# Kernel optimization log

Hardware: AMD Instinct MI355X
Metric: run time of the kernel (lower is better)

## Reference

```python
import jax, jax.numpy as jnp
import numpy as np


def _squash_global(v):
    # Faithful to torch: v.norm() with no dim -> global Frobenius norm (scalar).
    n2 = jnp.sum(v * v)
    n = jnp.sqrt(n2)
    scale = n2 / (1.0 + n2)
    return scale * v / n


def setup_inputs() -> dict:
    key = jax.random.key(0)
    k1, k2 = jax.random.split(key)
    B, R, Ci = 128, 1152, 8
    C, O = 10, 16
    x = jax.random.normal(k1, (B, R, Ci), dtype=jnp.float32)
    W = jax.random.normal(k2, (C, R, Ci, O), dtype=jnp.float32)  # routing_weights ~ randn
    return {"x": x, "W": W, "num_iterations": 3}


def reference(x, W, num_iterations):
    # prediction_vectors: [C, B, R, 1, O]
    u = jnp.einsum('bri,crio->cbro', x, W)[:, :, :, None, :]
    logits = jnp.zeros_like(u)
    v = None
    for _ in range(num_iterations):
        # batch_softmax: cat over dim0 + legacy softmax(dim=1 of 4D) == softmax over
        # the num_route_nodes axis (axis 2 here).
        c = jax.nn.softmax(logits, axis=2)
        s = jnp.sum(c * u, axis=2, keepdims=True)  # [C, B, 1, 1, O]
        v = _squash_global(s)
        logits = logits + u * v
    return v
```

## Files before the change

### kernel.cpp

```cpp
#include <hip/hip_runtime.h>
#include <math.h>

#define Bn   128
#define Rn   1152
#define CIn  8
#define Cn   10
#define On   16
#define BO   2048
#define CBO  20480
#define RC   12
#define NSEG 96
#define PSEG 24

__global__ __launch_bounds__(256)
void transpose_x(const float* __restrict__ X, float* __restrict__ XT)
{
    const int r = blockIdx.x;
    const int b = threadIdx.x & 127;
    const int g = threadIdx.x >> 7;
    float4 v = *(const float4*)(X + (size_t)b * (Rn * CIn) + r * CIn + g * 4);
    ((float4*)XT)[r * 256 + g * 128 + b] = v;
}

template<int PASS>
__global__ __launch_bounds__(256, 3)
void pass_kernel(const float* __restrict__ XT, const float* __restrict__ W,
                 const float* __restrict__ Sprev, const float* __restrict__ N2,
                 float* __restrict__ PT, float* __restrict__ PL)
{
    __shared__ __align__(16) float smem[4 * 64 * 34];
    float (*wlds)[128] = (float (*)[128])smem;
    float (*red)[64][34] = (float (*)[64][34])smem;

    const int blk  = blockIdx.x;
    const int c    = blk / 48;
    const int rem  = blk - c * 48;
    const int bh   = rem / 24;
    const int segq = rem - bh * 24;
    const int tid  = threadIdx.x;
    const int w    = tid >> 6;
    const int lane = tid & 63;
    const int b    = bh * 64 + lane;

    {
        const float4* gw4 = (const float4*)(W + (size_t)(c * Rn + segq * 48) * 128);
        float4* sw4 = (float4*)&wlds[0][0];
        #pragma unroll
        for (int k = 0; k < 6; ++k)
            sw4[tid + k * 256] = gw4[tid + k * 256];
    }

    float vs[16];
    if (PASS > 1) {
        float coef[PASS];
        #pragma unroll
        for (int t = 0; t < PASS - 1; ++t) {
            const float n2 = N2[t];
            coef[t] = n2 / ((1.0f + n2) * sqrtf(n2)) * 1.4426950408889634f;
        }
        const float* sp = Sprev + c * BO + b * On;
        #pragma unroll
        for (int q = 0; q < 4; ++q) {
            float4 a = make_float4(0.f, 0.f, 0.f, 0.f);
            #pragma unroll
            for (int t = 0; t < PASS - 1; ++t) {
                const float4 s4 = *(const float4*)(sp + t * CBO + q * 4);
                a.x = fmaf(coef[t], s4.x, a.x);
                a.y = fmaf(coef[t], s4.y, a.y);
                a.z = fmaf(coef[t], s4.z, a.z);
                a.w = fmaf(coef[t], s4.w, a.w);
            }
            vs[q * 4 + 0] = a.x; vs[q * 4 + 1] = a.y;
            vs[q * 4 + 2] = a.z; vs[q * 4 + 3] = a.w;
        }
    }

    float tacc[16], lacc[16];
    #pragma unroll
    for (int o = 0; o < 16; ++o) { tacc[o] = 0.0f; lacc[o] = 0.0f; }

    __syncthreads();

    const float4* XT4 = (const float4*)XT;
    for (int rr = 0; rr < RC; ++rr) {
        const int lrow = w * RC + rr;
        const int r    = segq * 48 + lrow;
        const float4 xa = XT4[r * 256 + b];
        const float4 xb = XT4[r * 256 + 128 + b];
        const float xi[8] = { xa.x, xa.y, xa.z, xa.w, xb.x, xb.y, xb.z, xb.w };

        float u[16];
        #pragma unroll
        for (int o = 0; o < 16; ++o) u[o] = 0.0f;
        #pragma unroll
        for (int i = 0; i < 8; ++i) {
            const float4 w0 = *(const float4*)&wlds[lrow][i * 16 + 0];
            const float4 w1 = *(const float4*)&wlds[lrow][i * 16 + 4];
            const float4 w2 = *(const float4*)&wlds[lrow][i * 16 + 8];
            const float4 w3 = *(const float4*)&wlds[lrow][i * 16 + 12];
            const float x = xi[i];
            u[0]  = fmaf(x, w0.x, u[0]);  u[1]  = fmaf(x, w0.y, u[1]);
            u[2]  = fmaf(x, w0.z, u[2]);  u[3]  = fmaf(x, w0.w, u[3]);
            u[4]  = fmaf(x, w1.x, u[4]);  u[5]  = fmaf(x, w1.y, u[5]);
            u[6]  = fmaf(x, w1.z, u[6]);  u[7]  = fmaf(x, w1.w, u[7]);
            u[8]  = fmaf(x, w2.x, u[8]);  u[9]  = fmaf(x, w2.y, u[9]);
            u[10] = fmaf(x, w2.z, u[10]); u[11] = fmaf(x, w2.w, u[11]);
            u[12] = fmaf(x, w3.x, u[12]); u[13] = fmaf(x, w3.y, u[13]);
            u[14] = fmaf(x, w3.z, u[14]); u[15] = fmaf(x, w3.w, u[15]);
        }
        #pragma unroll
        for (int o = 0; o < 16; ++o) {
            if (PASS == 1) {
                tacc[o] += u[o];
            } else {
                const float e = exp2f(u[o] * vs[o]);
                lacc[o] += e;
                tacc[o] = fmaf(e, u[o], tacc[o]);
            }
        }
    }

    __syncthreads();

    #pragma unroll
    for (int o = 0; o < 16; ++o) {
        red[w][lane][o]      = tacc[o];
        red[w][lane][16 + o] = lacc[o];
    }
    __syncthreads();

    {
        const int bl = tid >> 2;
        const int og = tid & 3;
        const int bg = bh * 64 + bl;
        float4 tv, lv;
        float* tp = (float*)&tv;
        float* lp = (float*)&lv;
        #pragma unroll
        for (int q = 0; q < 4; ++q) {
            const int o = og * 4 + q;
            tp[q] = red[0][bl][o] + red[1][bl][o] + red[2][bl][o] + red[3][bl][o];
            lp[q] = red[0][bl][16 + o] + red[1][bl][16 + o] +
                    red[2][bl][16 + o] + red[3][bl][16 + o];
        }
        const int idx = segq * CBO + c * BO + bg * On + og * 4;
        *(float4*)(PT + idx) = tv;
        if (PASS > 1) *(float4*)(PL + idx) = lv;
    }
}

template<int PASS>
__global__ __launch_bounds__(256)
void combine_kernel(const float* __restrict__ PT, const float* __restrict__ PL,
                    float* __restrict__ Sout, float* __restrict__ n2out)
{
    const int i = blockIdx.x * 256 + threadIdx.x;
    float T = 0.0f, L = 0.0f;
    #pragma unroll
    for (int s = 0; s < PSEG; ++s) T += PT[s * CBO + i];
    if (PASS == 1) {
        L = (float)Rn;
    } else {
        #pragma unroll
        for (int s = 0; s < PSEG; ++s) L += PL[s * CBO + i];
    }
    const float sv = T / L;
    Sout[i] = sv;
    float sq = sv * sv;
    #pragma unroll
    for (int d = 1; d < 64; d <<= 1) sq += __shfl_xor(sq, d);
    __shared__ float red[4];
    if ((threadIdx.x & 63) == 0) red[threadIdx.x >> 6] = sq;
    __syncthreads();
    if (threadIdx.x == 0)
        atomicAdd(n2out, red[0] + red[1] + red[2] + red[3]);
}

__global__ __launch_bounds__(256)
void final_kernel(const float* __restrict__ S, const float* __restrict__ n2p,
                  float* __restrict__ out)
{
    const int i = blockIdx.x * 256 + threadIdx.x;
    const float n2 = *n2p;
    const float coef = n2 / ((1.0f + n2) * sqrtf(n2));
    out[i] = coef * S[i];
}

extern "C" void kernel_launch(void* const* d_in, const int* in_sizes, int n_in,
                              void* d_out, int out_size, void* d_ws, size_t ws_size,
                              hipStream_t stream)
{
    const float* X = (const float*)d_in[0];
    const float* W = (const float*)d_in[1];
    float* ws = (float*)d_ws;
    float* XT = ws;
    float* N2 = XT + Rn * Bn * CIn;
    float* PT = N2 + 4;
    float* PL = PT + PSEG * CBO;
    float* S  = PL + PSEG * CBO;

    hipMemsetAsync(N2, 0, 16, stream);

    transpose_x<<<Rn, 256, 0, stream>>>(X, XT);
    pass_kernel<1><<<480, 256, 0, stream>>>(XT, W, S, N2, PT, PL);
    combine_kernel<1><<<80, 256, 0, stream>>>(PT, PL, S + 0 * CBO, N2 + 0);
    pass_kernel<2><<<480, 256, 0, stream>>>(XT, W, S, N2, PT, PL);
    combine_kernel<2><<<80, 256, 0, stream>>>(PT, PL, S + 1 * CBO, N2 + 1);
    pass_kernel<3><<<480, 256, 0, stream>>>(XT, W, S, N2, PT, PL);
    combine_kernel<3><<<80, 256, 0, stream>>>(PT, PL, S + 2 * CBO, N2 + 2);
    final_kernel<<<80, 256, 0, stream>>>(S + 2 * CBO, N2 + 2, (float*)d_out);
}
```

Before: 125.7 us.

## Fuse all routing passes into one persistent kernel with grid barriers

Replaces the eight separate launches (transpose, three pass/combine pairs, final scale) with one persistent kernel of 240 blocks × 512 threads that uses atomic-counter grid barriers between phases. Each block now covers 96 routing rows with 8 waves, which halves the partial-sum segments and adds a two-step LDS reduction. The aim is to remove kernel launch gaps and tail effects. In exchange it relies on all 240 blocks being co-resident for the spin barriers, and only 40 blocks do work in the combine phases.

```diff
diff --git a/kernel.cpp b/kernel.cpp
--- a/kernel.cpp
+++ b/kernel.cpp
@@ -9,45 +9,47 @@
 #define BO   2048
 #define CBO  20480
 #define RC   12
-#define NSEG 96
-#define PSEG 24
-
-__global__ __launch_bounds__(256)
-void transpose_x(const float* __restrict__ X, float* __restrict__ XT)
-{
-    const int r = blockIdx.x;
-    const int b = threadIdx.x & 127;
-    const int g = threadIdx.x >> 7;
-    float4 v = *(const float4*)(X + (size_t)b * (Rn * CIn) + r * CIn + g * 4);
-    ((float4*)XT)[r * 256 + g * 128 + b] = v;
+#define PSEG 12
+#define GRID 240
+#define NTHR 512
+#define AGT  __HIP_MEMORY_SCOPE_AGENT
+
+__device__ __forceinline__ void gbar(unsigned* bar, int tid)
+{
+    __syncthreads();
+    if (tid == 0) {
+        __hip_atomic_fetch_add(bar, 1u, __ATOMIC_RELEASE, AGT);
+        while (__hip_atomic_load(bar, __ATOMIC_RELAXED, AGT) < (unsigned)GRID)
+            __builtin_amdgcn_s_sleep(2);
+    }
+    __syncthreads();
+    __builtin_amdgcn_fence(__ATOMIC_ACQUIRE, "agent");
 }
 
 template<int PASS>
-__global__ __launch_bounds__(256, 3)
-void pass_kernel(const float* __restrict__ XT, const float* __restrict__ W,
-                 const float* __restrict__ Sprev, const float* __restrict__ N2,
-                 float* __restrict__ PT, float* __restrict__ PL)
-{
-    __shared__ __align__(16) float smem[4 * 64 * 34];
-    float (*wlds)[128] = (float (*)[128])smem;
+__device__ __forceinline__ void pass_phase(
+    int blk, int tid,
+    const float* __restrict__ XT, const float* __restrict__ W,
+    const float* __restrict__ Sprev, float* __restrict__ N2,
+    float* __restrict__ PT, float* __restrict__ PL, float* smem)
+{
+    float (*wlds)[128]   = (float (*)[128])smem;
     float (*red)[64][34] = (float (*)[64][34])smem;
 
-    const int blk  = blockIdx.x;
-    const int c    = blk / 48;
-    const int rem  = blk - c * 48;
-    const int bh   = rem / 24;
-    const int segq = rem - bh * 24;
-    const int tid  = threadIdx.x;
+    const int c    = blk / 24;
+    const int rem  = blk - c * 24;
+    const int bh   = rem / 12;
+    const int segq = rem - bh * 12;
     const int w    = tid >> 6;
     const int lane = tid & 63;
     const int b    = bh * 64 + lane;
 
     {
-        const float4* gw4 = (const float4*)(W + (size_t)(c * Rn + segq * 48) * 128);
-        float4* sw4 = (float4*)&wlds[0][0];
+        const float4* gw4 = (const float4*)(W + (size_t)(c * Rn + segq * 96) * 128);
+        float4* sw4 = (float4*)smem;
         #pragma unroll
         for (int k = 0; k < 6; ++k)
-            sw4[tid + k * 256] = gw4[tid + k * 256];
+            sw4[tid + k * 512] = gw4[tid + k * 512];
     }
 
     float vs[16];
@@ -55,7 +57,7 @@
         float coef[PASS];
         #pragma unroll
         for (int t = 0; t < PASS - 1; ++t) {
-            const float n2 = N2[t];
+            const float n2 = __hip_atomic_load(&N2[t], __ATOMIC_RELAXED, AGT);
             coef[t] = n2 / ((1.0f + n2) * sqrtf(n2)) * 1.4426950408889634f;
         }
         const float* sp = Sprev + c * BO + b * On;
@@ -84,7 +86,7 @@
     const float4* XT4 = (const float4*)XT;
     for (int rr = 0; rr < RC; ++rr) {
         const int lrow = w * RC + rr;
-        const int r    = segq * 48 + lrow;
+        const int r    = segq * 96 + lrow;
         const float4 xa = XT4[r * 256 + b];
         const float4 xb = XT4[r * 256 + 128 + b];
         const float xi[8] = { xa.x, xa.y, xa.z, xa.w, xb.x, xb.y, xb.z, xb.w };
@@ -122,39 +124,49 @@
 
     __syncthreads();
 
-    #pragma unroll
-    for (int o = 0; o < 16; ++o) {
-        red[w][lane][o]      = tacc[o];
-        red[w][lane][16 + o] = lacc[o];
+    if (w < 4) {
+        #pragma unroll
+        for (int o = 0; o < 16; ++o) {
+            red[w][lane][o]      = tacc[o];
+            red[w][lane][16 + o] = lacc[o];
+        }
+    }
+    __syncthreads();
+    if (w >= 4) {
+        #pragma unroll
+        for (int o = 0; o < 16; ++o) {
+            red[w - 4][lane][o]      += tacc[o];
+            red[w - 4][lane][16 + o] += lacc[o];
+        }
     }
     __syncthreads();
 
     {
-        const int bl = tid >> 2;
-        const int og = tid & 3;
+        const int bl = tid >> 3;
+        const int og = tid & 7;
         const int bg = bh * 64 + bl;
-        float4 tv, lv;
+        float2 tv, lv;
         float* tp = (float*)&tv;
         float* lp = (float*)&lv;
         #pragma unroll
-        for (int q = 0; q < 4; ++q) {
-            const int o = og * 4 + q;
+        for (int q = 0; q < 2; ++q) {
+            const int o = og * 2 + q;
             tp[q] = red[0][bl][o] + red[1][bl][o] + red[2][bl][o] + red[3][bl][o];
             lp[q] = red[0][bl][16 + o] + red[1][bl][16 + o] +
                     red[2][bl][16 + o] + red[3][bl][16 + o];
         }
-        const int idx = segq * CBO + c * BO + bg * On + og * 4;
-        *(float4*)(PT + idx) = tv;
-        if (PASS > 1) *(float4*)(PL + idx) = lv;
+        const int idx = segq * CBO + c * BO + bg * On + og * 2;
+        *(float2*)(PT + idx) = tv;
+        if (PASS > 1) *(float2*)(PL + idx) = lv;
     }
 }
 
 template<int PASS>
-__global__ __launch_bounds__(256)
-void combine_kernel(const float* __restrict__ PT, const float* __restrict__ PL,
-                    float* __restrict__ Sout, float* __restrict__ n2out)
-{
-    const int i = blockIdx.x * 256 + threadIdx.x;
+__device__ __forceinline__ void combine_phase(
+    int blk, int tid, const float* __restrict__ PT, const float* __restrict__ PL,
+    float* __restrict__ Sout, float* __restrict__ n2out, float* smem)
+{
+    const int i = blk * NTHR + tid;
     float T = 0.0f, L = 0.0f;
     #pragma unroll
     for (int s = 0; s < PSEG; ++s) T += PT[s * CBO + i];
@@ -169,21 +181,59 @@
     float sq = sv * sv;
     #pragma unroll
     for (int d = 1; d < 64; d <<= 1) sq += __shfl_xor(sq, d);
-    __shared__ float red[4];
-    if ((threadIdx.x & 63) == 0) red[threadIdx.x >> 6] = sq;
-    __syncthreads();
-    if (threadIdx.x == 0)
-        atomicAdd(n2out, red[0] + red[1] + red[2] + red[3]);
-}
-
-__global__ __launch_bounds__(256)
-void final_kernel(const float* __restrict__ S, const float* __restrict__ n2p,
+    if ((tid & 63) == 0) smem[tid >> 6] = sq;
+    __syncthreads();
+    if (tid == 0) {
+        float s8 = 0.0f;
+        #pragma unroll
+        for (int k = 0; k < 8; ++k) s8 += smem[k];
+        atomicAdd(n2out, s8);
+    }
+}
+
+__global__ __launch_bounds__(NTHR, 1)
+void fused_kernel(const float* __restrict__ X, const float* __restrict__ W,
+                  float* __restrict__ XT, float* __restrict__ PT,
+                  float* __restrict__ PL, float* __restrict__ S,
+                  float* __restrict__ N2, unsigned* __restrict__ BAR,
                   float* __restrict__ out)
 {
-    const int i = blockIdx.x * 256 + threadIdx.x;
-    const float n2 = *n2p;
-    const float coef = n2 / ((1.0f + n2) * sqrtf(n2));
-    out[i] = coef * S[i];
+    __shared__ __align__(16) float smem[96 * 128];
+
+    const int blk = blockIdx.x;
+    const int tid = threadIdx.x;
+
+    for (int idx = blk * NTHR + tid; idx < Rn * 256; idx += GRID * NTHR) {
+        const int r = idx >> 8;
+        const int j = idx & 255;
+        const int b = j & 127;
+        const int g = j >> 7;
+        float4 v = *(const float4*)(X + (size_t)b * (Rn * CIn) + r * CIn + g * 4);
+        ((float4*)XT)[r * 256 + g * 128 + b] = v;
+    }
+    gbar(BAR + 0, tid);
+
+    pass_phase<1>(blk, tid, XT, W, S, N2, PT, PL, smem);
+    gbar(BAR + 1, tid);
+    if (blk < 40) combine_phase<1>(blk, tid, PT, PL, S + 0 * CBO, N2 + 0, smem);
+    gbar(BAR + 2, tid);
+
+    pass_phase<2>(blk, tid, XT, W, S, N2, PT, PL, smem);
+    gbar(BAR + 3, tid);
+    if (blk < 40) combine_phase<2>(blk, tid, PT, PL, S + 1 * CBO, N2 + 1, smem);
+    gbar(BAR + 4, tid);
+
+    pass_phase<3>(blk, tid, XT, W, S, N2, PT, PL, smem);
+    gbar(BAR + 5, tid);
+    if (blk < 40) combine_phase<3>(blk, tid, PT, PL, S + 2 * CBO, N2 + 2, smem);
+    gbar(BAR + 6, tid);
+
+    if (blk < 40) {
+        const int i = blk * NTHR + tid;
+        const float n2 = __hip_atomic_load(&N2[2], __ATOMIC_RELAXED, AGT);
+        const float coef = n2 / ((1.0f + n2) * sqrtf(n2));
+        out[i] = coef * S[2 * CBO + i];
+    }
 }
 
 extern "C" void kernel_launch(void* const* d_in, const int* in_sizes, int n_in,
@@ -193,20 +243,15 @@
     const float* X = (const float*)d_in[0];
     const float* W = (const float*)d_in[1];
     float* ws = (float*)d_ws;
-    float* XT = ws;
-    float* N2 = XT + Rn * Bn * CIn;
-    float* PT = N2 + 4;
-    float* PL = PT + PSEG * CBO;
-    float* S  = PL + PSEG * CBO;
-
-    hipMemsetAsync(N2, 0, 16, stream);
-
-    transpose_x<<<Rn, 256, 0, stream>>>(X, XT);
-    pass_kernel<1><<<480, 256, 0, stream>>>(XT, W, S, N2, PT, PL);
-    combine_kernel<1><<<80, 256, 0, stream>>>(PT, PL, S + 0 * CBO, N2 + 0);
-    pass_kernel<2><<<480, 256, 0, stream>>>(XT, W, S, N2, PT, PL);
-    combine_kernel<2><<<80, 256, 0, stream>>>(PT, PL, S + 1 * CBO, N2 + 1);
-    pass_kernel<3><<<480, 256, 0, stream>>>(XT, W, S, N2, PT, PL);
-    combine_kernel<3><<<80, 256, 0, stream>>>(PT, PL, S + 2 * CBO, N2 + 2);
-    final_kernel<<<80, 256, 0, stream>>>(S + 2 * CBO, N2 + 2, (float*)d_out);
-}
+    float* XT  = ws;
+    float* N2  = XT + Rn * Bn * CIn;
+    unsigned* BAR = (unsigned*)(N2 + 4);
+    float* PT  = N2 + 12;
+    float* PL  = PT + PSEG * CBO;
+    float* S   = PL + PSEG * CBO;
+    float* out = (float*)d_out;
+
+    hipMemsetAsync(N2, 0, 48, stream);
+
+    fused_kernel<<<GRID, NTHR, 0, stream>>>(X, W, XT, PT, PL, S, N2, BAR, out);
+}
```

Result: slower. 300.5 us (+139.1%).

## Fuse combine and final kernels into pass kernels via atomics and ticket

Applied to the files above, without the earlier changes.

The per-segment partial buffers and the separate combine and final kernels are replaced. Each pass block now atomically adds its reduced T/L sums straight into one global accumulator per pass. Each later pass recomputes the squared norms redundantly in every block, and the last block of pass 3 (chosen with a ticket counter) writes the squashed output. The memset is folded into the transpose kernel, and the x loads are software-prefetched one row ahead. This removes four launches and the partial-sum round trips, at the cost of atomic contention, a redundant 20K-element norm scan in every block, and a serial tail in the final block.

```diff
diff --git a/kernel.cpp b/kernel.cpp
--- a/kernel.cpp
+++ b/kernel.cpp
@@ -9,28 +9,41 @@
 #define BO   2048
 #define CBO  20480
 #define RC   12
-#define NSEG 96
-#define PSEG 24
+#define GRID 480
+#define LOG2E 1.4426950408889634f
+#define INV_R 8.6805555e-4f
+
 
 __global__ __launch_bounds__(256)
-void transpose_x(const float* __restrict__ X, float* __restrict__ XT)
+void transpose_x(const float* __restrict__ X, float* __restrict__ XT,
+                 float* __restrict__ TL)
 {
     const int r = blockIdx.x;
     const int b = threadIdx.x & 127;
     const int g = threadIdx.x >> 7;
     float4 v = *(const float4*)(X + (size_t)b * (Rn * CIn) + r * CIn + g * 4);
     ((float4*)XT)[r * 256 + g * 128 + b] = v;
+    const int zi = blockIdx.x * 256 + threadIdx.x;
+    if (zi < 25604) ((float4*)TL)[zi] = make_float4(0.f, 0.f, 0.f, 0.f);
 }
 
 template<int PASS>
-__global__ __launch_bounds__(256, 3)
+__global__ __launch_bounds__(256, 2)
 void pass_kernel(const float* __restrict__ XT, const float* __restrict__ W,
-                 const float* __restrict__ Sprev, const float* __restrict__ N2,
-                 float* __restrict__ PT, float* __restrict__ PL)
+                 float* __restrict__ TL, float* __restrict__ out)
 {
     __shared__ __align__(16) float smem[4 * 64 * 34];
-    float (*wlds)[128] = (float (*)[128])smem;
+    __shared__ float sred[8];
+    __shared__ int sdone;
+    float (*wlds)[128]   = (float (*)[128])smem;
     float (*red)[64][34] = (float (*)[64][34])smem;
+
+    float* T1 = TL;
+    float* T2 = TL + CBO;
+    float* L2 = TL + 2 * CBO;
+    float* T3 = TL + 3 * CBO;
+    float* L3 = TL + 4 * CBO;
+    unsigned* ticket = (unsigned*)(TL + 5 * CBO);
 
     const int blk  = blockIdx.x;
     const int c    = blk / 48;
@@ -44,7 +57,7 @@
 
     {
         const float4* gw4 = (const float4*)(W + (size_t)(c * Rn + segq * 48) * 128);
-        float4* sw4 = (float4*)&wlds[0][0];
+        float4* sw4 = (float4*)smem;
         #pragma unroll
         for (int k = 0; k < 6; ++k)
             sw4[tid + k * 256] = gw4[tid + k * 256];
@@ -52,26 +65,59 @@
 
     float vs[16];
     if (PASS > 1) {
-        float coef[PASS];
-        #pragma unroll
-        for (int t = 0; t < PASS - 1; ++t) {
-            const float n2 = N2[t];
-            coef[t] = n2 / ((1.0f + n2) * sqrtf(n2)) * 1.4426950408889634f;
-        }
-        const float* sp = Sprev + c * BO + b * On;
-        #pragma unroll
-        for (int q = 0; q < 4; ++q) {
-            float4 a = make_float4(0.f, 0.f, 0.f, 0.f);
+        float n2a = 0.f, n2b = 0.f;
+        const float4* T1v = (const float4*)T1;
+        if (PASS == 2) {
+            for (int i = tid; i < 5120; i += 256) {
+                float4 v = T1v[i];
+                v.x *= INV_R; v.y *= INV_R; v.z *= INV_R; v.w *= INV_R;
+                n2a += v.x * v.x + v.y * v.y + v.z * v.z + v.w * v.w;
+            }
+        } else {
+            const float4* T2v = (const float4*)T2;
+            const float4* L2v = (const float4*)L2;
+            for (int i = tid; i < 5120; i += 256) {
+                float4 v = T1v[i];
+                v.x *= INV_R; v.y *= INV_R; v.z *= INV_R; v.w *= INV_R;
+                n2a += v.x * v.x + v.y * v.y + v.z * v.z + v.w * v.w;
+                float4 t = T2v[i], l = L2v[i];
+                float s0 = t.x / l.x, s1 = t.y / l.y, s2 = t.z / l.z, s3 = t.w / l.w;
+                n2b += s0 * s0 + s1 * s1 + s2 * s2 + s3 * s3;
+            }
+        }
+        #pragma unroll
+        for (int d = 1; d < 64; d <<= 1) {
+            n2a += __shfl_xor(n2a, d);
+            n2b += __shfl_xor(n2b, d);
+        }
+        if (lane == 0) { sred[w] = n2a; sred[4 + w] = n2b; }
+        __syncthreads();
+        n2a = sred[0] + sred[1] + sred[2] + sred[3];
+        n2b = sred[4] + sred[5] + sred[6] + sred[7];
+
+        const float c1 = n2a / ((1.f + n2a) * sqrtf(n2a)) * (LOG2E * INV_R);
+        const float* s1p = T1 + c * BO + b * On;
+        if (PASS == 2) {
             #pragma unroll
-            for (int t = 0; t < PASS - 1; ++t) {
-                const float4 s4 = *(const float4*)(sp + t * CBO + q * 4);
-                a.x = fmaf(coef[t], s4.x, a.x);
-                a.y = fmaf(coef[t], s4.y, a.y);
-                a.z = fmaf(coef[t], s4.z, a.z);
-                a.w = fmaf(coef[t], s4.w, a.w);
-            }
-            vs[q * 4 + 0] = a.x; vs[q * 4 + 1] = a.y;
-            vs[q * 4 + 2] = a.z; vs[q * 4 + 3] = a.w;
+            for (int q = 0; q < 4; ++q) {
+                float4 v = *(const float4*)(s1p + q * 4);
+                vs[q*4+0] = c1 * v.x; vs[q*4+1] = c1 * v.y;
+                vs[q*4+2] = c1 * v.z; vs[q*4+3] = c1 * v.w;
+            }
+        } else {
+            const float c2 = n2b / ((1.f + n2b) * sqrtf(n2b)) * LOG2E;
+            const float* t2p = T2 + c * BO + b * On;
+            const float* l2p = L2 + c * BO + b * On;
+            #pragma unroll
+            for (int q = 0; q < 4; ++q) {
+                float4 v = *(const float4*)(s1p + q * 4);
+                float4 t = *(const float4*)(t2p + q * 4);
+                float4 l = *(const float4*)(l2p + q * 4);
+                vs[q*4+0] = c1 * v.x + c2 * (t.x / l.x);
+                vs[q*4+1] = c1 * v.y + c2 * (t.y / l.y);
+                vs[q*4+2] = c1 * v.z + c2 * (t.z / l.z);
+                vs[q*4+3] = c1 * v.w + c2 * (t.w / l.w);
+            }
         }
     }
 
@@ -82,11 +128,16 @@
     __syncthreads();
 
     const float4* XT4 = (const float4*)XT;
+    const float4* xp  = XT4 + (size_t)(segq * 48 + w * RC) * 256 + b;
+    float4 xa = xp[0];
+    float4 xb = xp[128];
     for (int rr = 0; rr < RC; ++rr) {
+        float4 na = xa, nb = xb;
+        if (rr + 1 < RC) {
+            na = xp[(rr + 1) * 256];
+            nb = xp[(rr + 1) * 256 + 128];
+        }
         const int lrow = w * RC + rr;
-        const int r    = segq * 48 + lrow;
-        const float4 xa = XT4[r * 256 + b];
-        const float4 xb = XT4[r * 256 + 128 + b];
         const float xi[8] = { xa.x, xa.y, xa.z, xa.w, xb.x, xb.y, xb.z, xb.w };
 
         float u[16];
@@ -118,14 +169,15 @@
                 tacc[o] = fmaf(e, u[o], tacc[o]);
             }
         }
+        xa = na; xb = nb;
     }
 
     __syncthreads();
 
     #pragma unroll
     for (int o = 0; o < 16; ++o) {
-        red[w][lane][o]      = tacc[o];
-        red[w][lane][16 + o] = lacc[o];
+        red[w][lane][o] = tacc[o];
+        if (PASS > 1) red[w][lane][16 + o] = lacc[o];
     }
     __syncthreads();
 
@@ -133,57 +185,53 @@
         const int bl = tid >> 2;
         const int og = tid & 3;
         const int bg = bh * 64 + bl;
-        float4 tv, lv;
-        float* tp = (float*)&tv;
-        float* lp = (float*)&lv;
+        float* Tslot = (PASS == 1) ? T1 : (PASS == 2) ? T2 : T3;
+        float* Lslot = (PASS == 2) ? L2 : L3;
+        const int idx = c * BO + bg * On + og * 4;
         #pragma unroll
         for (int q = 0; q < 4; ++q) {
             const int o = og * 4 + q;
-            tp[q] = red[0][bl][o] + red[1][bl][o] + red[2][bl][o] + red[3][bl][o];
-            lp[q] = red[0][bl][16 + o] + red[1][bl][16 + o] +
-                    red[2][bl][16 + o] + red[3][bl][16 + o];
-        }
-        const int idx = segq * CBO + c * BO + bg * On + og * 4;
-        *(float4*)(PT + idx) = tv;
-        if (PASS > 1) *(float4*)(PL + idx) = lv;
-    }
-}
-
-template<int PASS>
-__global__ __launch_bounds__(256)
-void combine_kernel(const float* __restrict__ PT, const float* __restrict__ PL,
-                    float* __restrict__ Sout, float* __restrict__ n2out)
-{
-    const int i = blockIdx.x * 256 + threadIdx.x;
-    float T = 0.0f, L = 0.0f;
-    #pragma unroll
-    for (int s = 0; s < PSEG; ++s) T += PT[s * CBO + i];
-    if (PASS == 1) {
-        L = (float)Rn;
-    } else {
-        #pragma unroll
-        for (int s = 0; s < PSEG; ++s) L += PL[s * CBO + i];
-    }
-    const float sv = T / L;
-    Sout[i] = sv;
-    float sq = sv * sv;
-    #pragma unroll
-    for (int d = 1; d < 64; d <<= 1) sq += __shfl_xor(sq, d);
-    __shared__ float red[4];
-    if ((threadIdx.x & 63) == 0) red[threadIdx.x >> 6] = sq;
-    __syncthreads();
-    if (threadIdx.x == 0)
-        atomicAdd(n2out, red[0] + red[1] + red[2] + red[3]);
-}
-
-__global__ __launch_bounds__(256)
-void final_kernel(const float* __restrict__ S, const float* __restrict__ n2p,
-                  float* __restrict__ out)
-{
-    const int i = blockIdx.x * 256 + threadIdx.x;
-    const float n2 = *n2p;
-    const float coef = n2 / ((1.0f + n2) * sqrtf(n2));
-    out[i] = coef * S[i];
+            atomicAdd(Tslot + idx + q,
+                      red[0][bl][o] + red[1][bl][o] + red[2][bl][o] + red[3][bl][o]);
+            if (PASS > 1)
+                atomicAdd(Lslot + idx + q,
+                          red[0][bl][16+o] + red[1][bl][16+o] +
+                          red[2][bl][16+o] + red[3][bl][16+o]);
+        }
+    }
+
+    if (PASS == 3) {
+        __syncthreads();
+        if (tid == 0) {
+            __threadfence();
+            sdone = (atomicAdd(ticket, 1u) == GRID - 1);
+        }
+        __syncthreads();
+        if (sdone) {
+            __threadfence();
+            const float4* T3v = (const float4*)T3;
+            const float4* L3v = (const float4*)L3;
+            float acc = 0.f;
+            for (int i = tid; i < 5120; i += 256) {
+                float4 t = T3v[i], l = L3v[i];
+                float s0 = t.x / l.x, s1 = t.y / l.y, s2 = t.z / l.z, s3 = t.w / l.w;
+                acc += s0 * s0 + s1 * s1 + s2 * s2 + s3 * s3;
+            }
+            #pragma unroll
+            for (int d = 1; d < 64; d <<= 1) acc += __shfl_xor(acc, d);
+            if (lane == 0) sred[w] = acc;
+            __syncthreads();
+            const float n2 = sred[0] + sred[1] + sred[2] + sred[3];
+            const float c3 = n2 / ((1.f + n2) * sqrtf(n2));
+            for (int i = tid; i < 5120; i += 256) {
+                float4 t = T3v[i], l = L3v[i];
+                float4 o4;
+                o4.x = c3 * t.x / l.x; o4.y = c3 * t.y / l.y;
+                o4.z = c3 * t.z / l.z; o4.w = c3 * t.w / l.w;
+                ((float4*)out)[i] = o4;
+            }
+        }
+    }
 }
 
 extern "C" void kernel_launch(void* const* d_in, const int* in_sizes, int n_in,
@@ -194,19 +242,11 @@
     const float* W = (const float*)d_in[1];
     float* ws = (float*)d_ws;
     float* XT = ws;
-    float* N2 = XT + Rn * Bn * CIn;
-    float* PT = N2 + 4;
-    float* PL = PT + PSEG * CBO;
-    float* S  = PL + PSEG * CBO;
-
-    hipMemsetAsync(N2, 0, 16, stream);
-
-    transpose_x<<<Rn, 256, 0, stream>>>(X, XT);
-    pass_kernel<1><<<480, 256, 0, stream>>>(XT, W, S, N2, PT, PL);
-    combine_kernel<1><<<80, 256, 0, stream>>>(PT, PL, S + 0 * CBO, N2 + 0);
-    pass_kernel<2><<<480, 256, 0, stream>>>(XT, W, S, N2, PT, PL);
-    combine_kernel<2><<<80, 256, 0, stream>>>(PT, PL, S + 1 * CBO, N2 + 1);
-    pass_kernel<3><<<480, 256, 0, stream>>>(XT, W, S, N2, PT, PL);
-    combine_kernel<3><<<80, 256, 0, stream>>>(PT, PL, S + 2 * CBO, N2 + 2);
-    final_kernel<<<80, 256, 0, stream>>>(S + 2 * CBO, N2 + 2, (float*)d_out);
+    float* TL = XT + Rn * Bn * CIn;
+    float* out = (float*)d_out;
+
+    transpose_x<<<Rn, 256, 0, stream>>>(X, XT, TL);
+    pass_kernel<1><<<GRID, 256, 0, stream>>>(XT, W, TL, out);
+    pass_kernel<2><<<GRID, 256, 0, stream>>>(XT, W, TL, out);
+    pass_kernel<3><<<GRID, 256, 0, stream>>>(XT, W, TL, out);
 }
```

New measurement: 161.1 us. 1.28x slower.
